# Kernel tuning notes

Hardware: AMD Instinct MI355X
Metric: run time of the kernel (lower is better)

Reference implementation:

```python
import jax, jax.numpy as jnp
import numpy as np

N, E, K, D = 100000, 3200000, 1024, 11


def setup_inputs() -> dict:
    key = jax.random.key(0)
    ks = jax.random.split(key, 11)
    return {
        "x": jax.random.normal(ks[0], (N, D), jnp.float32),
        "edge_index": jax.random.randint(ks[1], (2, E), 0, N, dtype=jnp.int32),
        "ready_idx": jnp.sort(jax.random.randint(ks[2], (K,), 0, N, dtype=jnp.int32)),
        "W1": jax.random.normal(ks[3], (D, 64), jnp.float32) * 0.2,
        "b1": jax.random.normal(ks[4], (64,), jnp.float32) * 0.02,
        "W2": jax.random.normal(ks[5], (75, 1), jnp.float32) * 0.2,
        "b2": jax.random.normal(ks[6], (1,), jnp.float32) * 0.02,
        "Wd": jax.random.normal(ks[7], (64, 1), jnp.float32) * 0.2,
        "bd": jax.random.normal(ks[8], (1,), jnp.float32) * 0.02,
        "Wv": jax.random.normal(ks[9], (64, 1), jnp.float32) * 0.2,
        "bv": jax.random.normal(ks[10], (1,), jnp.float32) * 0.02,
    }


def gcn_conv(x, W, b, src, dst):
    """PyG GCNConv with flow='target_to_source': gather from dst, aggregate at src.
    Symmetric normalization with self-loops (weight 1)."""
    n = x.shape[0]
    h = x @ W  # [N, F_out]
    loop = jnp.arange(n, dtype=src.dtype)
    s = jnp.concatenate([src, loop])  # aggregation index (row for target_to_source)
    d = jnp.concatenate([dst, loop])  # gather index
    deg = jax.ops.segment_sum(jnp.ones(s.shape, h.dtype), s, num_segments=n)
    dis = jnp.where(deg > 0, jax.lax.rsqrt(jnp.maximum(deg, 1e-12)), 0.0)
    norm = dis[s] * dis[d]  # [E+N]
    out = jax.ops.segment_sum(norm[:, None] * h[d], s, num_segments=n)
    return out + b


def reference(x, edge_index, ready_idx, W1, b1, W2, b2, Wd, bd, Wv, bv):
    src, dst = edge_index[0], edge_index[1]
    h = jax.nn.relu(gcn_conv(x, W1, b1, src, dst))           # [N, 64]
    x_input = jnp.concatenate([h, x], axis=1)                # [N, 75]
    probs_n = gcn_conv(x_input, W2, b2, src, dst)            # [N, 1]
    x_mean = jnp.mean(h, axis=0)                             # [64]
    v = x_mean @ Wv + bv                                     # [1]
    prob_nothing = x_mean @ Wd + bd                          # [1]
    logits = jnp.concatenate([probs_n[ready_idx, 0], prob_nothing])  # [K+1]
    probs = jax.nn.softmax(logits)
    return probs, v
```

## Files before the change

kernel.cpp:

```cpp
#include <hip/hip_runtime.h>
#include <hip/hip_fp16.h>
#include <math.h>

#define N_ 100000
#define E_ 3200000
#define K_ 1024
#define D_ 11
#define NBUCK_ 391
#define NPAD_ (NBUCK_ * 256)
#define CAPB_ 16384
#define CAP_ 32
#define CAPW_ 33
#define GB_ 512
#define BT_ 1024
#define CHUNK_ 6256
#define XC_ 32
#define RSEG_ 4096
#define RSTRIDE_ 16

static inline size_t align512(size_t x) { return (x + 511) & ~(size_t)511; }

__device__ inline float2 h2f(unsigned int u) {
    __half2 h = *reinterpret_cast<__half2*>(&u);
    return __half22float2(h);
}

__global__ __launch_bounds__(BT_) void k_bin(const int* __restrict__ src,
                                             const int* __restrict__ dst,
                                             int* __restrict__ bcur,
                                             int* __restrict__ gbuf) {
    __shared__ int sbuf[NBUCK_ * CAPW_];
    __shared__ int scnt[NBUCK_];
    int t = threadIdx.x;
    for (int b = t; b < NBUCK_; b += BT_) scnt[b] = 0;
    __syncthreads();
    long e0 = (long)blockIdx.x * CHUNK_;
    for (int r = 0; r < CHUNK_; r += BT_ * 8) {
        int off = r + t * 8;
        long i0 = e0 + off;
        if (off < CHUNK_ && i0 + 7 < E_) {
            int4 s0 = *(const int4*)(src + i0);
            int4 s1 = *(const int4*)(src + i0 + 4);
            int4 d0 = *(const int4*)(dst + i0);
            int4 d1 = *(const int4*)(dst + i0 + 4);
            int ss[8] = {s0.x, s0.y, s0.z, s0.w, s1.x, s1.y, s1.z, s1.w};
            int dd[8] = {d0.x, d0.y, d0.z, d0.w, d1.x, d1.y, d1.z, d1.w};
#pragma unroll
            for (int q = 0; q < 8; q++) {
                int b = ss[q] >> 8;
                int pack = ((ss[q] & 255) << 17) | dd[q];
                int pos = atomicAdd(&scnt[b], 1);
                if (pos < CAP_) sbuf[b * CAPW_ + pos] = pack;
                else gbuf[b * CAPB_ + atomicAdd(&bcur[b], 1)] = pack;
            }
        }
    }
    __syncthreads();
    for (int b = t; b < NBUCK_; b += BT_) {
        int c = min(scnt[b], CAP_);
        while (c >= 16) {
            int off = atomicAdd(&bcur[b], 16);
            int g = b * CAPB_ + off;
            c -= 16;
            if ((off & 3) == 0) {
                int4* gp = (int4*)(gbuf + g);
#pragma unroll
                for (int q = 0; q < 4; q++)
                    gp[q] = make_int4(sbuf[b*CAPW_ + c + 4*q],
                                      sbuf[b*CAPW_ + c + 4*q + 1],
                                      sbuf[b*CAPW_ + c + 4*q + 2],
                                      sbuf[b*CAPW_ + c + 4*q + 3]);
            } else {
                for (int k = 0; k < 16; k++) gbuf[g + k] = sbuf[b*CAPW_ + c + k];
            }
        }
        if (c > 0) {
            int g = b * CAPB_ + atomicAdd(&bcur[b], c);
            for (int k = 0; k < c; k++) gbuf[g + k] = sbuf[b*CAPW_ + k];
        }
    }
}

__global__ __launch_bounds__(1024) void k_deg(const int* __restrict__ bcur,
                                              const int* __restrict__ gbuf,
                                              const float* __restrict__ x,
                                              const int* __restrict__ ready,
                                              float* __restrict__ dis,
                                              __half* __restrict__ xh,
                                              unsigned char* __restrict__ flag,
                                              float* __restrict__ pr_raw,
                                              float* __restrict__ xpart,
                                              int* __restrict__ rcntp) {
    __shared__ int hist[256];
    int t = threadIdx.x, b = blockIdx.x;
    if (t < 256) hist[t] = 0;
    int gi = b * 1024 + t;
    if (gi < XC_ * 64) xpart[gi] = 0.f;
    if (gi < 32 * RSTRIDE_) rcntp[gi] = 0;
    __syncthreads();
    int base = b * CAPB_;
    int cnt = min(bcur[b], CAPB_);
    int p = t * 4;
    for (; p + 3 < cnt; p += 4096) {
        int4 v = *(const int4*)(gbuf + base + p);
        atomicAdd(&hist[v.x >> 17], 1);
        atomicAdd(&hist[v.y >> 17], 1);
        atomicAdd(&hist[v.z >> 17], 1);
        atomicAdd(&hist[v.w >> 17], 1);
    }
    if (p < cnt) {
        for (int q = p; q < cnt; q++) atomicAdd(&hist[gbuf[base + q] >> 17], 1);
    }
    __syncthreads();
    if (t < 256) {
        int node = (b << 8) + t;
        if (node < N_) {
            float dv = rsqrtf((float)(hist[t] + 1));
            dis[node] = dv;
            pr_raw[node] = 0.f;
            __half hh[16];
#pragma unroll
            for (int j = 0; j < D_; j++)
                hh[j] = __float2half_rn(x[(size_t)node * D_ + j]);
            hh[11] = __float2half_rn(dv);
#pragma unroll
            for (int j = 12; j < 16; j++) hh[j] = __float2half_rn(0.f);
            uint4* dst = (uint4*)(xh + (size_t)node * 16);
            dst[0] = *(uint4*)(hh);
            dst[1] = *(uint4*)(hh + 8);
            int lo = 0, hi = K_ - 1, f = 0;
            while (lo <= hi) {
                int mid = (lo + hi) >> 1;
                int v = ready[mid];
                if (v == node) { f = 1; break; }
                if (v < node) lo = mid + 1; else hi = mid - 1;
            }
            flag[node] = (unsigned char)f;
        }
    }
}

__global__ __launch_bounds__(1024, 8) void k_agx(
    const int* __restrict__ bcur, const int* __restrict__ gbuf,
    const __half* __restrict__ xh, const float* __restrict__ x,
    const unsigned char* __restrict__ flag,
    const float* __restrict__ W1, const float* __restrict__ b1,
    const float* __restrict__ W2,
    float* __restrict__ hd, float* __restrict__ xpart,
    int* __restrict__ rcntp, int2* __restrict__ redge) {
    __shared__ int sorted[CAPB_];
    __shared__ int hist[256];
    __shared__ int incl[256];
    __shared__ int offa[256];
    __shared__ int cur[256];
    __shared__ float sW1[D_ * 64];
    __shared__ float sb1[64];
    __shared__ float sW2[75];
    __shared__ float smean[64];
    int t = threadIdx.x, b = blockIdx.x;
    if (t < D_ * 64) sW1[t] = W1[t];
    if (t >= 768 && t < 832) { sb1[t - 768] = b1[t - 768]; smean[t - 768] = 0.f; }
    if (t >= 832 && t < 907) sW2[t - 832] = W2[t - 832];
    if (t < 256) hist[t] = 0;
    __syncthreads();
    int base = b * CAPB_;
    int cnt = min(bcur[b], CAPB_);
    for (int idx = t; idx < cnt; idx += 1024)
        atomicAdd(&hist[gbuf[base + idx] >> 17], 1);
    __syncthreads();
    if (t < 256) incl[t] = hist[t];
    __syncthreads();
    for (int off = 1; off < 256; off <<= 1) {
        int v = 0;
        if (t < 256 && t >= off) v = incl[t - off];
        __syncthreads();
        if (t < 256) incl[t] += v;
        __syncthreads();
    }
    if (t < 256) { int o = incl[t] - hist[t]; offa[t] = o; cur[t] = o; }
    __syncthreads();
    for (int idx = t; idx < cnt; idx += 1024) {
        int pk = gbuf[base + idx];
        sorted[atomicAdd(&cur[pk >> 17], 1)] = pk;
    }
    __syncthreads();
    int nl = t >> 2, q = t & 3;
    int node = (b << 8) + nl;
    bool valid = node < N_;
    int my_start = offa[nl], my_cnt = hist[nl];
    const uint4* xr4 = (const uint4*)xh;
    float acc[D_];
#pragma unroll
    for (int j = 0; j < D_; j++) acc[j] = 0.f;
    for (int i = q; i < my_cnt; i += 4) {
        int pack = sorted[my_start + i];
        size_t r = (size_t)(pack & 131071) * 2;
        uint4 A = xr4[r], B = xr4[r + 1];
        float2 f0 = h2f(A.x), f1 = h2f(A.y), f2 = h2f(A.z);
        float2 f3 = h2f(A.w), f4 = h2f(B.x), f5 = h2f(B.y);
        float w = f5.y;
        acc[0]  = fmaf(w, f0.x, acc[0]);
        acc[1]  = fmaf(w, f0.y, acc[1]);
        acc[2]  = fmaf(w, f1.x, acc[2]);
        acc[3]  = fmaf(w, f1.y, acc[3]);
        acc[4]  = fmaf(w, f2.x, acc[4]);
        acc[5]  = fmaf(w, f2.y, acc[5]);
        acc[6]  = fmaf(w, f3.x, acc[6]);
        acc[7]  = fmaf(w, f3.y, acc[7]);
        acc[8]  = fmaf(w, f4.x, acc[8]);
        acc[9]  = fmaf(w, f4.y, acc[9]);
        acc[10] = fmaf(w, f5.x, acc[10]);
    }
#pragma unroll
    for (int j = 0; j < D_; j++) {
        acc[j] += __shfl_xor(acc[j], 1);
        acc[j] += __shfl_xor(acc[j], 2);
    }
    float hreg[16];
    float h2v = 0.f;
    float di = 0.f;
    if (valid) {
        di = rsqrtf((float)(hist[nl] + 1));
        float xr_[D_], g[D_];
#pragma unroll
        for (int j = 0; j < D_; j++) xr_[j] = x[(size_t)node * D_ + j];
        if (q == 0) {
#pragma unroll
            for (int jj = 0; jj < D_; jj++) h2v = fmaf(xr_[jj], sW2[64 + jj], h2v);
        }
#pragma unroll
        for (int j = 0; j < D_; j++) g[j] = di * (acc[j] + di * xr_[j]);
        int fbase = q << 4;
#pragma unroll
        for (int j = 0; j < 16; j++) {
            int f = fbase + j;
            float a = sb1[f];
#pragma unroll
            for (int jj = 0; jj < D_; jj++) a = fmaf(g[jj], sW1[jj * 64 + f], a);
            float hf = fmaxf(a, 0.f);
            hreg[j] = hf;
            h2v = fmaf(hf, sW2[f], h2v);
        }
    } else {
#pragma unroll
        for (int j = 0; j < 16; j++) hreg[j] = 0.f;
    }
    h2v += __shfl_xor(h2v, 1);
    h2v += __shfl_xor(h2v, 2);
    if (valid && q == 0) hd[node] = di * h2v;

    int lane = t & 63;
#pragma unroll
    for (int j = 0; j < 16; j++) {
        float v = hreg[j];
        v += __shfl_xor(v, 4);
        v += __shfl_xor(v, 8);
        v += __shfl_xor(v, 16);
        v += __shfl_xor(v, 32);
        if (lane < 4) atomicAdd(&smean[(lane << 4) + j], v);
    }
    __syncthreads();
    if (t < 64) atomicAdd(&xpart[((b & (XC_ - 1)) << 6) + t], smean[t]);

    if (valid && my_cnt > 0 && flag[node]) {
        int r = b & 31;
        int slot = 0;
        if (q == 0) slot = atomicAdd(&rcntp[r * RSTRIDE_], my_cnt);
        slot = __shfl(slot, lane & ~3);
        int lim = min(my_cnt, max(0, RSEG_ - slot));
        for (int i2 = q; i2 < lim; i2 += 4)
            redge[(r << 12) + slot + i2] =
                make_int2(node, sorted[my_start + i2] & 131071);
    }
}

__global__ void k_pr(const int* __restrict__ rcntp, const int2* __restrict__ redge,
                     const float* __restrict__ hd, float* __restrict__ pr_raw) {
    int idx = blockIdx.x * blockDim.x + threadIdx.x;
    int r = idx >> 12;
    int off = idx & (RSEG_ - 1);
    if (r < 32 && off < min(rcntp[r * RSTRIDE_], RSEG_)) {
        int2 e = redge[(r << 12) + off];
        atomicAdd(&pr_raw[e.x], hd[e.y]);
    }
}

__global__ __launch_bounds__(1024) void k_final(
    const int* __restrict__ ready, const float* __restrict__ dis,
    const float* __restrict__ hd, const float* __restrict__ pr_raw,
    const float* __restrict__ xpart,
    const float* __restrict__ b2,
    const float* __restrict__ Wd, const float* __restrict__ bd,
    const float* __restrict__ Wv, const float* __restrict__ bv,
    float* __restrict__ out) {
    __shared__ float xm[64];
    __shared__ float red[1024];
    __shared__ float s_max, s_sum, s_pn, s_v;
    int t = threadIdx.x;
    if (t < 64) {
        float s = 0.f;
#pragma unroll
        for (int c = 0; c < XC_; c++) s += xpart[(c << 6) + t];
        xm[t] = s * (1.0f / N_);
    }
    __syncthreads();
    if (t == 0) {
        float pn = bd[0], vv = bv[0];
        for (int f = 0; f < 64; f++) { pn += xm[f] * Wd[f]; vv += xm[f] * Wv[f]; }
        s_pn = pn; s_v = vv;
    }
    int r = ready[t];
    float dr = dis[r];
    float l = dr * (pr_raw[r] + hd[r]) + b2[0];
    __syncthreads();
    float pn = s_pn;
    red[t] = (t == 0) ? fmaxf(l, pn) : l;
    __syncthreads();
    for (int sft = 512; sft > 0; sft >>= 1) {
        if (t < sft) red[t] = fmaxf(red[t], red[t + sft]);
        __syncthreads();
    }
    if (t == 0) s_max = red[0];
    __syncthreads();
    float m = s_max;
    float el = expf(l - m);
    red[t] = el + ((t == 0) ? expf(pn - m) : 0.f);
    __syncthreads();
    for (int sft = 512; sft > 0; sft >>= 1) {
        if (t < sft) red[t] += red[t + sft];
        __syncthreads();
    }
    if (t == 0) s_sum = red[0];
    __syncthreads();
    float inv = 1.0f / s_sum;
    out[t] = el * inv;
    if (t == 0) {
        out[K_] = expf(pn - m) * inv;
        out[K_ + 1] = s_v;
    }
}

extern "C" void kernel_launch(void* const* d_in, const int* in_sizes, int n_in,
                              void* d_out, int out_size, void* d_ws, size_t ws_size,
                              hipStream_t stream) {
    const float* x    = (const float*)d_in[0];
    const int*   ei   = (const int*)d_in[1];
    const int*   src  = ei;
    const int*   dst  = ei + E_;
    const int*   ready= (const int*)d_in[2];
    const float* W1   = (const float*)d_in[3];
    const float* b1   = (const float*)d_in[4];
    const float* W2   = (const float*)d_in[5];
    const float* b2   = (const float*)d_in[6];
    const float* Wd   = (const float*)d_in[7];
    const float* bd   = (const float*)d_in[8];
    const float* Wv   = (const float*)d_in[9];
    const float* bv   = (const float*)d_in[10];
    float* out = (float*)d_out;

    char* ws = (char*)d_ws;
    size_t o = 0;
    int*   bcur   = (int*)(ws + o);          o += align512(NBUCK_ * sizeof(int));
    int*   rcntp  = (int*)(ws + o);          o += align512(32 * RSTRIDE_ * sizeof(int));
    int*   gbuf   = (int*)(ws + o);          o += align512((size_t)NBUCK_ * CAPB_ * sizeof(int));
    __half* xh    = (__half*)(ws + o);       o += align512((size_t)N_ * 16 * sizeof(__half));
    int2*  redge  = (int2*)(ws + o);         o += align512((size_t)32 * RSEG_ * sizeof(int2));
    float* dis    = (float*)(ws + o);        o += align512(N_ * sizeof(float));
    float* hd     = (float*)(ws + o);        o += align512(N_ * sizeof(float));
    float* pr_raw = (float*)(ws + o);        o += align512(N_ * sizeof(float));
    unsigned char* flag = (unsigned char*)(ws + o); o += align512(N_);
    float* xpart  = (float*)(ws + o);        o += align512(XC_ * 64 * sizeof(float));

    const int B = 256;
    int g_pr = (32 * RSEG_) / B;

    hipMemsetAsync(bcur, 0, NBUCK_ * sizeof(int), stream);
    k_bin  <<<GB_, BT_, 0, stream>>>(src, dst, bcur, gbuf);
    k_deg  <<<NBUCK_, 1024, 0, stream>>>(bcur, gbuf, x, ready, dis, xh, flag,
                                         pr_raw, xpart, rcntp);
    k_agx  <<<NBUCK_, 1024, 0, stream>>>(bcur, gbuf, xh, x, flag, W1, b1, W2,
                                         hd, xpart, rcntp, redge);
    k_pr   <<<g_pr, B, 0, stream>>>(rcntp, redge, hd, pr_raw);
    k_final<<<1, 1024, 0, stream>>>(ready, dis, hd, pr_raw, xpart,
                                    b2, Wd, bd, Wv, bv, out);
}
```

Measured before the change: 186.8 us.

## Fuse degree and aggregation kernels using a grid-wide spin barrier

Merges the degree/histogram kernel into the aggregation kernel, so each block builds its bucket histogram once and reuses it for both the dis/xh setup and the local counting sort. A global atomic counter barrier replaces the kernel boundary, making all xh/dis writes visible before the neighbour gathers start. This removes one launch and one re-read of the bucket buffer. In exchange it relies on all 391 blocks of 1024 threads being co-resident, or the spin barrier deadlocks.

```diff
diff --git a/kernel.cpp b/kernel.cpp
--- a/kernel.cpp
+++ b/kernel.cpp
@@ -7,7 +7,6 @@
 #define K_ 1024
 #define D_ 11
 #define NBUCK_ 391
-#define NPAD_ (NBUCK_ * 256)
 #define CAPB_ 16384
 #define CAP_ 32
 #define CAPW_ 33
@@ -17,6 +16,7 @@
 #define XC_ 32
 #define RSEG_ 4096
 #define RSTRIDE_ 16
+#define BAROFF_ 448
 
 static inline size_t align512(size_t x) { return (x + 511) & ~(size_t)511; }
 
@@ -81,73 +81,16 @@
     }
 }
 
-__global__ __launch_bounds__(1024) void k_deg(const int* __restrict__ bcur,
-                                              const int* __restrict__ gbuf,
-                                              const float* __restrict__ x,
-                                              const int* __restrict__ ready,
-                                              float* __restrict__ dis,
-                                              __half* __restrict__ xh,
-                                              unsigned char* __restrict__ flag,
-                                              float* __restrict__ pr_raw,
-                                              float* __restrict__ xpart,
-                                              int* __restrict__ rcntp) {
-    __shared__ int hist[256];
-    int t = threadIdx.x, b = blockIdx.x;
-    if (t < 256) hist[t] = 0;
-    int gi = b * 1024 + t;
-    if (gi < XC_ * 64) xpart[gi] = 0.f;
-    if (gi < 32 * RSTRIDE_) rcntp[gi] = 0;
-    __syncthreads();
-    int base = b * CAPB_;
-    int cnt = min(bcur[b], CAPB_);
-    int p = t * 4;
-    for (; p + 3 < cnt; p += 4096) {
-        int4 v = *(const int4*)(gbuf + base + p);
-        atomicAdd(&hist[v.x >> 17], 1);
-        atomicAdd(&hist[v.y >> 17], 1);
-        atomicAdd(&hist[v.z >> 17], 1);
-        atomicAdd(&hist[v.w >> 17], 1);
-    }
-    if (p < cnt) {
-        for (int q = p; q < cnt; q++) atomicAdd(&hist[gbuf[base + q] >> 17], 1);
-    }
-    __syncthreads();
-    if (t < 256) {
-        int node = (b << 8) + t;
-        if (node < N_) {
-            float dv = rsqrtf((float)(hist[t] + 1));
-            dis[node] = dv;
-            pr_raw[node] = 0.f;
-            __half hh[16];
-#pragma unroll
-            for (int j = 0; j < D_; j++)
-                hh[j] = __float2half_rn(x[(size_t)node * D_ + j]);
-            hh[11] = __float2half_rn(dv);
-#pragma unroll
-            for (int j = 12; j < 16; j++) hh[j] = __float2half_rn(0.f);
-            uint4* dst = (uint4*)(xh + (size_t)node * 16);
-            dst[0] = *(uint4*)(hh);
-            dst[1] = *(uint4*)(hh + 8);
-            int lo = 0, hi = K_ - 1, f = 0;
-            while (lo <= hi) {
-                int mid = (lo + hi) >> 1;
-                int v = ready[mid];
-                if (v == node) { f = 1; break; }
-                if (v < node) lo = mid + 1; else hi = mid - 1;
-            }
-            flag[node] = (unsigned char)f;
-        }
-    }
-}
-
-__global__ __launch_bounds__(1024, 8) void k_agx(
+__global__ __launch_bounds__(1024, 8) void k_fused(
     const int* __restrict__ bcur, const int* __restrict__ gbuf,
-    const __half* __restrict__ xh, const float* __restrict__ x,
-    const unsigned char* __restrict__ flag,
+    const float* __restrict__ x, const int* __restrict__ ready,
     const float* __restrict__ W1, const float* __restrict__ b1,
     const float* __restrict__ W2,
-    float* __restrict__ hd, float* __restrict__ xpart,
-    int* __restrict__ rcntp, int2* __restrict__ redge) {
+    float* __restrict__ dis, __half* __restrict__ xh,
+    unsigned char* __restrict__ flag, float* __restrict__ pr_raw,
+    float* __restrict__ xpart, int* __restrict__ rcntp,
+    float* __restrict__ hd, int2* __restrict__ redge,
+    int* __restrict__ bar) {
     __shared__ int sorted[CAPB_];
     __shared__ int hist[256];
     __shared__ int incl[256];
@@ -162,13 +105,51 @@
     if (t >= 768 && t < 832) { sb1[t - 768] = b1[t - 768]; smean[t - 768] = 0.f; }
     if (t >= 832 && t < 907) sW2[t - 832] = W2[t - 832];
     if (t < 256) hist[t] = 0;
+    int gi = b * 1024 + t;
+    if (gi < XC_ * 64) xpart[gi] = 0.f;
+    if (gi < 32 * RSTRIDE_) rcntp[gi] = 0;
     __syncthreads();
     int base = b * CAPB_;
     int cnt = min(bcur[b], CAPB_);
-    for (int idx = t; idx < cnt; idx += 1024)
-        atomicAdd(&hist[gbuf[base + idx] >> 17], 1);
-    __syncthreads();
-    if (t < 256) incl[t] = hist[t];
+    int p = t * 4;
+    for (; p + 3 < cnt; p += 4096) {
+        int4 v = *(const int4*)(gbuf + base + p);
+        atomicAdd(&hist[v.x >> 17], 1);
+        atomicAdd(&hist[v.y >> 17], 1);
+        atomicAdd(&hist[v.z >> 17], 1);
+        atomicAdd(&hist[v.w >> 17], 1);
+    }
+    if (p < cnt) {
+        for (int q = p; q < cnt; q++) atomicAdd(&hist[gbuf[base + q] >> 17], 1);
+    }
+    __syncthreads();
+    if (t < 256) {
+        int node = (b << 8) + t;
+        if (node < N_) {
+            float dv = rsqrtf((float)(hist[t] + 1));
+            dis[node] = dv;
+            pr_raw[node] = 0.f;
+            __half hh[16];
+#pragma unroll
+            for (int j = 0; j < D_; j++)
+                hh[j] = __float2half_rn(x[(size_t)node * D_ + j]);
+            hh[11] = __float2half_rn(dv);
+#pragma unroll
+            for (int j = 12; j < 16; j++) hh[j] = __float2half_rn(0.f);
+            uint4* dst = (uint4*)(xh + (size_t)node * 16);
+            dst[0] = *(uint4*)(hh);
+            dst[1] = *(uint4*)(hh + 8);
+            int lo = 0, hi = K_ - 1, f = 0;
+            while (lo <= hi) {
+                int mid = (lo + hi) >> 1;
+                int v = ready[mid];
+                if (v == node) { f = 1; break; }
+                if (v < node) lo = mid + 1; else hi = mid - 1;
+            }
+            flag[node] = (unsigned char)f;
+        }
+        incl[t] = hist[t];
+    }
     __syncthreads();
     for (int off = 1; off < 256; off <<= 1) {
         int v = 0;
@@ -182,6 +163,16 @@
     for (int idx = t; idx < cnt; idx += 1024) {
         int pk = gbuf[base + idx];
         sorted[atomicAdd(&cur[pk >> 17], 1)] = pk;
+    }
+    __syncthreads();
+    if (t == 0) {
+        __threadfence();
+        atomicAdd(bar, 1);
+        while (__hip_atomic_load(bar, __ATOMIC_RELAXED,
+                                 __HIP_MEMORY_SCOPE_AGENT) < NBUCK_) {
+            __builtin_amdgcn_s_sleep(2);
+        }
+        __threadfence();
     }
     __syncthreads();
     int nl = t >> 2, q = t & 3;
@@ -360,7 +351,8 @@
 
     char* ws = (char*)d_ws;
     size_t o = 0;
-    int*   bcur   = (int*)(ws + o);          o += align512(NBUCK_ * sizeof(int));
+    int*   bcur   = (int*)(ws + o);          o += align512(512 * sizeof(int));
+    int*   bar    = bcur + BAROFF_;
     int*   rcntp  = (int*)(ws + o);          o += align512(32 * RSTRIDE_ * sizeof(int));
     int*   gbuf   = (int*)(ws + o);          o += align512((size_t)NBUCK_ * CAPB_ * sizeof(int));
     __half* xh    = (__half*)(ws + o);       o += align512((size_t)N_ * 16 * sizeof(__half));
@@ -374,12 +366,11 @@
     const int B = 256;
     int g_pr = (32 * RSEG_) / B;
 
-    hipMemsetAsync(bcur, 0, NBUCK_ * sizeof(int), stream);
+    hipMemsetAsync(bcur, 0, 512 * sizeof(int), stream);
     k_bin  <<<GB_, BT_, 0, stream>>>(src, dst, bcur, gbuf);
-    k_deg  <<<NBUCK_, 1024, 0, stream>>>(bcur, gbuf, x, ready, dis, xh, flag,
-                                         pr_raw, xpart, rcntp);
-    k_agx  <<<NBUCK_, 1024, 0, stream>>>(bcur, gbuf, xh, x, flag, W1, b1, W2,
-                                         hd, xpart, rcntp, redge);
+    k_fused<<<NBUCK_, 1024, 0, stream>>>(bcur, gbuf, x, ready, W1, b1, W2,
+                                         dis, xh, flag, pr_raw, xpart, rcntp,
+                                         hd, redge, bar);
     k_pr   <<<g_pr, B, 0, stream>>>(rcntp, redge, hd, pr_raw);
     k_final<<<1, 1024, 0, stream>>>(ready, dis, hd, pr_raw, xpart,
                                     b2, Wd, bd, Wv, bv, out);
```

After: 216.5 us. +15.9%, slower.
